# Kernel tuning notes

Measured on AMD Instinct MI355X. Metric: run time of the kernel, lower is better.

Reference implementation:

```python
import math
import jax, jax.numpy as jnp
import numpy as np

B, L, D = 2, 2048, 1024
NH = 16
HS = D // NH
BLOCK_SIZE = 2048


def setup_inputs() -> dict:
    key = jax.random.key(0)
    ks = jax.random.split(key, 4)
    x = jax.random.normal(ks[0], (B, L, D), dtype=jnp.float32)
    Wqkv = jax.random.normal(ks[1], (D, 3 * D), dtype=jnp.float32) * 0.02
    bqkv = jnp.zeros((3 * D,), dtype=jnp.float32)
    Wproj = jax.random.normal(ks[2], (D, D), dtype=jnp.float32) * 0.02
    bproj = jnp.zeros((D,), dtype=jnp.float32)
    Er = jax.random.normal(ks[3], (BLOCK_SIZE, HS), dtype=jnp.float32)
    return {"x": x, "Wqkv": Wqkv, "bqkv": bqkv, "Wproj": Wproj, "bproj": bproj, "Er": Er}


def _skew(QEr):
    # QEr: [B, nh, L, L]  (Music Transformer skew trick)
    b, nh, nr, nc = QEr.shape
    padded = jnp.pad(QEr, ((0, 0), (0, 0), (0, 0), (1, 0)))  # [B, nh, nr, nc+1]
    reshaped = padded.reshape(b, nh, nc + 1, nr)
    return reshaped[:, :, 1:, :]  # [B, nh, nr, nc]


def reference(x, Wqkv, bqkv, Wproj, bproj, Er):
    b, l, d = x.shape
    qkv = x @ Wqkv + bqkv  # [B, L, 3D]
    q, k, v = jnp.split(qkv, 3, axis=2)
    q = q.reshape(b, l, NH, HS).transpose(0, 2, 1, 3)  # [B, nh, L, hs]
    k = k.reshape(b, l, NH, HS).transpose(0, 2, 1, 3)
    v = v.reshape(b, l, NH, HS).transpose(0, 2, 1, 3)

    start = BLOCK_SIZE - l
    Er_t = Er[start:, :].T  # [hs, L]
    QEr = jnp.einsum('bhld,dm->bhlm', q, Er_t)  # [B, nh, L, L]
    Srel = _skew(QEr)

    QK_t = jnp.einsum('bhld,bhmd->bhlm', q, k)
    scale = 1.0 / math.sqrt(HS)
    att = (QK_t + Srel) * scale
    causal = jnp.tril(jnp.ones((l, l), dtype=bool))
    att = jnp.where(causal[None, None, :, :], att, jnp.float32(-jnp.inf))
    att = jax.nn.softmax(att, axis=-1)
    y = jnp.einsum('bhlm,bhmd->bhld', att, v)
    y = y.transpose(0, 2, 1, 3).reshape(b, l, d)
    return y @ Wproj + bproj
```

## Files before the change

### kernel.cpp

```cpp
#include <hip/hip_runtime.h>
#include <stdint.h>

#define BB 2
#define LL 2048
#define DD 1024
#define NHH 16
#define HSS 64

typedef __bf16 bf16x8 __attribute__((ext_vector_type(8)));
typedef float f32x4 __attribute__((ext_vector_type(4)));

__device__ __forceinline__ bf16x8 load8(const float* p) {
  float4 f0 = *(const float4*)p;
  float4 f1 = *(const float4*)(p + 4);
  bf16x8 v;
  v[0] = (__bf16)f0.x; v[1] = (__bf16)f0.y; v[2] = (__bf16)f0.z; v[3] = (__bf16)f0.w;
  v[4] = (__bf16)f1.x; v[5] = (__bf16)f1.y; v[6] = (__bf16)f1.z; v[7] = (__bf16)f1.w;
  return v;
}
__device__ __forceinline__ bf16x8 load8(const __bf16* p) {
  return *(const bf16x8*)p;
}

__device__ __forceinline__ void async_ld16(__bf16* lds_uniform_base,
                                           const __bf16* gptr_per_lane) {
  __builtin_amdgcn_global_load_lds(
      (const __attribute__((address_space(1))) void*)gptr_per_lane,
      (__attribute__((address_space(3))) void*)lds_uniform_base, 16, 0, 0);
}

__global__ void prep_k(const float* __restrict__ Wqkv, const float* __restrict__ x,
                       const float* __restrict__ Er, __bf16* __restrict__ WqkvT,
                       __bf16* __restrict__ xb, __bf16* __restrict__ Erb) {
  int tx = threadIdx.x, ty = threadIdx.y;
  int tid = ty * 32 + tx;
  if (blockIdx.z == 1) {
    if (blockIdx.x >= 2048) return;
    size_t off = ((size_t)blockIdx.x * 256 + tid) * 8;
    *(bf16x8*)&xb[off] = load8(&x[off]);
    return;
  }
  if (blockIdx.z == 2) {
    if (blockIdx.x >= 64) return;
    size_t off = ((size_t)blockIdx.x * 256 + tid) * 8;
    *(bf16x8*)&Erb[off] = load8(&Er[off]);
    return;
  }
  __shared__ __bf16 tile[32][33];
  int c0 = (blockIdx.x % 96) * 32, r0 = (blockIdx.x / 96) * 32;
#pragma unroll
  for (int i = ty; i < 32; i += 8)
    tile[i][tx] = (__bf16)Wqkv[(size_t)(r0 + i) * 3072 + c0 + tx];
  __syncthreads();
#pragma unroll
  for (int i = ty; i < 32; i += 8)
    WqkvT[(size_t)(c0 + i) * 1024 + r0 + tx] = tile[tx][i];
}

__global__ void tconv_k(const float* __restrict__ src, __bf16* __restrict__ dst,
                        int R, int C) {
  __shared__ __bf16 tile[32][33];
  int c0 = blockIdx.x * 32, r0 = blockIdx.y * 32;
  int tx = threadIdx.x, ty = threadIdx.y;
#pragma unroll
  for (int i = ty; i < 32; i += 8)
    tile[i][tx] = (__bf16)src[(size_t)(r0 + i) * C + c0 + tx];
  __syncthreads();
#pragma unroll
  for (int i = ty; i < 32; i += 8)
    dst[(size_t)(c0 + i) * R + r0 + tx] = tile[tx][i];
}

__global__ __launch_bounds__(256) void gemm_qkv_k(
    const __bf16* __restrict__ A, const __bf16* __restrict__ Bt,
    const float* __restrict__ bias, __bf16* __restrict__ Qo,
    __bf16* __restrict__ Ko, __bf16* __restrict__ Vto) {
  const int K = 1024;
  __shared__ __align__(16) __bf16 As[128 * 32];
  __shared__ __align__(16) __bf16 Bs[128 * 32];
  int t = threadIdx.x;
  int wave = t >> 6, lane = t & 63, qd = lane >> 4, lr = lane & 15;
  int m0 = blockIdx.y * 128, n0 = blockIdx.x * 128;
  int wm = (wave >> 1) * 64, wn = (wave & 1) * 64;
  f32x4 acc[4][4] = {};
  int srow = lane >> 2, sch = (lane & 3) * 8;
  const __bf16* Ab[2];
  const __bf16* Bb[2];
#pragma unroll
  for (int c = 0; c < 2; c++) {
    Ab[c] = A + (size_t)(m0 + (wave * 2 + c) * 16 + srow) * K + sch;
    Bb[c] = Bt + (size_t)(n0 + (wave * 2 + c) * 16 + srow) * K + sch;
  }
  for (int k0 = 0; k0 < K; k0 += 32) {
    __syncthreads();
#pragma unroll
    for (int c = 0; c < 2; c++) {
      async_ld16(&As[(wave * 2 + c) * 512], Ab[c] + k0);
      async_ld16(&Bs[(wave * 2 + c) * 512], Bb[c] + k0);
    }
    __syncthreads();
    bf16x8 af[4], bfr[4];
#pragma unroll
    for (int mt = 0; mt < 4; mt++)
      af[mt] = *(const bf16x8*)&As[(wm + mt * 16 + lr) * 32 + qd * 8];
#pragma unroll
    for (int nt = 0; nt < 4; nt++)
      bfr[nt] = *(const bf16x8*)&Bs[(wn + nt * 16 + lr) * 32 + qd * 8];
#pragma unroll
    for (int mt = 0; mt < 4; mt++)
#pragma unroll
      for (int nt = 0; nt < 4; nt++)
        acc[mt][nt] = __builtin_amdgcn_mfma_f32_16x16x32_bf16(af[mt], bfr[nt],
                                                              acc[mt][nt], 0, 0, 0);
  }
  float bvv[4];
#pragma unroll
  for (int nt = 0; nt < 4; nt++) bvv[nt] = bias[n0 + wn + nt * 16 + lr];
#pragma unroll
  for (int mt = 0; mt < 4; mt++)
#pragma unroll
    for (int nt = 0; nt < 4; nt++)
#pragma unroll
      for (int r = 0; r < 4; r++) {
        int row = m0 + wm + mt * 16 + qd * 4 + r;
        int col = n0 + wn + nt * 16 + lr;
        __bf16 bb = (__bf16)(acc[mt][nt][r] + bvv[nt]);
        int b = row >> 11, l = row & 2047;
        int h = (col >> 6) & 15, d = col & 63;
        if (col < DD) {
          Qo[(((size_t)(b * NHH + h)) * LL + l) * HSS + d] = bb;
        } else if (col < 2 * DD) {
          Ko[(((size_t)(b * NHH + h)) * LL + l) * HSS + d] = bb;
        } else {
          Vto[(((size_t)(b * NHH + h)) * HSS + d) * LL + l] = bb;
        }
      }
}

__global__ __launch_bounds__(256) void gemm_proj_k(
    const __bf16* __restrict__ A, const __bf16* __restrict__ Bt,
    const float* __restrict__ bias, float* __restrict__ out) {
  const int K = 1024, N = 1024;
  __shared__ __align__(16) __bf16 As[128 * 32];
  __shared__ __align__(16) __bf16 Bs[64 * 32];
  int t = threadIdx.x;
  int wave = t >> 6, lane = t & 63, qd = lane >> 4, lr = lane & 15;
  int m0 = blockIdx.y * 128, n0 = blockIdx.x * 64;
  int wm = (wave >> 1) * 64, wn = (wave & 1) * 32;
  f32x4 acc[4][2] = {};
  int srow = lane >> 2, sch = (lane & 3) * 8;
  const __bf16* Ab[2];
  const __bf16* Bb;
#pragma unroll
  for (int c = 0; c < 2; c++)
    Ab[c] = A + (size_t)(m0 + (wave * 2 + c) * 16 + srow) * K + sch;
  Bb = Bt + (size_t)(n0 + wave * 16 + srow) * K + sch;

  for (int k0 = 0; k0 < K; k0 += 32) {
    __syncthreads();
#pragma unroll
    for (int c = 0; c < 2; c++)
      async_ld16(&As[(wave * 2 + c) * 512], Ab[c] + k0);
    async_ld16(&Bs[wave * 512], Bb + k0);
    __syncthreads();
    bf16x8 af[4], bfr[2];
#pragma unroll
    for (int mt = 0; mt < 4; mt++)
      af[mt] = *(const bf16x8*)&As[(wm + mt * 16 + lr) * 32 + qd * 8];
#pragma unroll
    for (int nt = 0; nt < 2; nt++)
      bfr[nt] = *(const bf16x8*)&Bs[(wn + nt * 16 + lr) * 32 + qd * 8];
#pragma unroll
    for (int mt = 0; mt < 4; mt++)
#pragma unroll
      for (int nt = 0; nt < 2; nt++)
        acc[mt][nt] = __builtin_amdgcn_mfma_f32_16x16x32_bf16(af[mt], bfr[nt],
                                                              acc[mt][nt], 0, 0, 0);
  }
  float bvv[2];
#pragma unroll
  for (int nt = 0; nt < 2; nt++) bvv[nt] = bias[n0 + wn + nt * 16 + lr];
#pragma unroll
  for (int mt = 0; mt < 4; mt++)
#pragma unroll
    for (int nt = 0; nt < 2; nt++)
#pragma unroll
      for (int r = 0; r < 4; r++) {
        int row = m0 + wm + mt * 16 + qd * 4 + r;
        int col = n0 + wn + nt * 16 + lr;
        out[(size_t)row * N + col] = acc[mt][nt][r] + bvv[nt];
      }
}

__global__ __launch_bounds__(256, 3) void flash_k(
    const __bf16* __restrict__ Qg, const __bf16* __restrict__ Kg,
    const __bf16* __restrict__ Vtg, const __bf16* __restrict__ Erb,
    __bf16* __restrict__ Po0, __bf16* __restrict__ Po1,
    float* __restrict__ Lp0, float* __restrict__ Lp1) {
  __shared__ __align__(16) __bf16 Kld[64 * 72];
  __shared__ __align__(16) __bf16 Vld[64 * 72];
  __shared__ __align__(16) __bf16 Pball[4][16 * 72];

  int bh = blockIdx.x;
  int tile = 31 - (int)blockIdx.y;
  int i0 = tile * 64;
  int niter = tile + 1;
  int mid = (niter + 1) >> 1;
  int it0 = (blockIdx.z == 0) ? 0 : mid;
  int it1 = (blockIdx.z == 0) ? mid : niter;
  const __bf16* Qh = Qg + (size_t)bh * LL * HSS;
  const __bf16* Kh = Kg + (size_t)bh * LL * HSS;
  const __bf16* Vth = Vtg + (size_t)bh * HSS * LL;
  int b = bh >> 4, h = bh & 15;
  int t = threadIdx.x, wave = t >> 6, lane = t & 63, qd = lane >> 4, lr = lane & 15;
  __bf16* Pb = &Pball[wave][0];
  int cbase = 48 - wave * 16;

  bf16x8 bones;
#pragma unroll
  for (int q = 0; q < 8; q++) bones[q] = (lr == 0) ? (__bf16)1.f : (__bf16)0.f;

  int jj = t >> 2, hf = t & 3;

  bf16x8 aq[2];
  {
    const __bf16* qrow = Qh + (size_t)(i0 + wave * 16 + lr) * HSS + qd * 8;
    aq[0] = *(const bf16x8*)qrow;
    aq[1] = *(const bf16x8*)(qrow + 32);
  }
  f32x4 oacc[5] = {};

  bf16x8 kr0, kr1, vr0, vr1;
  auto prefetch = [&](int j0) {
    kr0 = *(const bf16x8*)&Kh[(size_t)(j0 + jj) * HSS + hf * 16];
    kr1 = *(const bf16x8*)&Kh[(size_t)(j0 + jj) * HSS + hf * 16 + 8];
    vr0 = *(const bf16x8*)&Vth[(size_t)jj * LL + j0 + hf * 16];
    vr1 = *(const bf16x8*)&Vth[(size_t)jj * LL + j0 + hf * 16 + 8];
  };
  if (it0 < it1) prefetch(it0 * 64);

  for (int it = it0; it < it1; ++it) {
    int j0 = it * 64;
    __syncthreads();
    *(bf16x8*)&Kld[jj * 72 + hf * 16] = kr0;
    *(bf16x8*)&Kld[jj * 72 + hf * 16 + 8] = kr1;
    *(bf16x8*)&Vld[jj * 72 + hf * 16] = vr0;
    *(bf16x8*)&Vld[jj * 72 + hf * 16 + 8] = vr1;
    __syncthreads();
    if (it + 1 < it1) prefetch((it + 1) * 64);

    bf16x8 ef[5][2];
    int ebase = LL - 64 - i0 + j0 + cbase;
#pragma unroll
    for (int ct = 0; ct < 5; ct++) {
      int e = ebase + ct * 16 + lr;
      e = (e < LL) ? e : (LL - 1);
#pragma unroll
      for (int kc = 0; kc < 2; kc++)
        ef[ct][kc] = *(const bf16x8*)&Erb[(size_t)e * HSS + kc * 32 + qd * 8];
    }

    f32x4 sacc[4] = {};
#pragma unroll
    for (int ct = 0; ct < 4; ct++)
#pragma unroll
      for (int kc = 0; kc < 2; kc++) {
        bf16x8 bk = *(const bf16x8*)&Kld[(ct * 16 + lr) * 72 + kc * 32 + qd * 8];
        sacc[ct] = __builtin_amdgcn_mfma_f32_16x16x32_bf16(aq[kc], bk, sacc[ct], 0, 0, 0);
      }
    f32x4 racc[5] = {};
#pragma unroll
    for (int ct = 0; ct < 5; ct++)
#pragma unroll
      for (int kc = 0; kc < 2; kc++)
        racc[ct] = __builtin_amdgcn_mfma_f32_16x16x32_bf16(aq[kc], ef[ct][kc],
                                                           racc[ct], 0, 0, 0);

#pragma unroll
    for (int r = 0; r < 4; r++) {
      int tr = qd * 4 + r;
      int base = 15 - tr + lr;
      int src = qd * 16 + (base & 15);
      int hi = base >> 4;
      float sh[5];
#pragma unroll
      for (int ct = 0; ct < 5; ct++) sh[ct] = __shfl(racc[ct][r], src, 64);
      int gi = i0 + wave * 16 + tr;
#pragma unroll
      for (int ct2 = 0; ct2 < 4; ct2++) {
        float rel = hi ? sh[ct2 + 1] : sh[ct2];
        float s = (sacc[ct2][r] + rel) * 0.125f;
        int gj = j0 + ct2 * 16 + lr;
        float p = (gj <= gi) ? __expf(s) : 0.f;
        Pb[tr * 72 + ct2 * 16 + lr] = (__bf16)p;
      }
    }

    bf16x8 ap0 = *(const bf16x8*)&Pb[lr * 72 + qd * 8];
    bf16x8 ap1 = *(const bf16x8*)&Pb[lr * 72 + 32 + qd * 8];
#pragma unroll
    for (int dt = 0; dt < 4; dt++) {
      bf16x8 bv0 = *(const bf16x8*)&Vld[(dt * 16 + lr) * 72 + qd * 8];
      bf16x8 bv1 = *(const bf16x8*)&Vld[(dt * 16 + lr) * 72 + 32 + qd * 8];
      oacc[dt] = __builtin_amdgcn_mfma_f32_16x16x32_bf16(ap0, bv0, oacc[dt], 0, 0, 0);
      oacc[dt] = __builtin_amdgcn_mfma_f32_16x16x32_bf16(ap1, bv1, oacc[dt], 0, 0, 0);
    }
    oacc[4] = __builtin_amdgcn_mfma_f32_16x16x32_bf16(ap0, bones, oacc[4], 0, 0, 0);
    oacc[4] = __builtin_amdgcn_mfma_f32_16x16x32_bf16(ap1, bones, oacc[4], 0, 0, 0);
  }

  __bf16* Po = (blockIdx.z == 0) ? Po0 : Po1;
  float* Lp = (blockIdx.z == 0) ? Lp0 : Lp1;
#pragma unroll
  for (int r = 0; r < 4; r++) {
    int l = i0 + wave * 16 + qd * 4 + r;
    if (lr == 0) Lp[(size_t)bh * LL + l] = oacc[4][r];
#pragma unroll
    for (int dt = 0; dt < 4; dt++) {
      int d = dt * 16 + lr;
      Po[((size_t)(b * LL) + l) * DD + h * HSS + d] = (__bf16)oacc[dt][r];
    }
  }
}

__global__ void combine_k(const __bf16* __restrict__ Po0,
                          const __bf16* __restrict__ Po1,
                          const float* __restrict__ Lp0,
                          const float* __restrict__ Lp1,
                          __bf16* __restrict__ Y) {
  size_t f = ((size_t)blockIdx.x * 256 + threadIdx.x) * 8;
  int dfull = (int)(f & 1023);
  int h = dfull >> 6;
  int l = (int)((f >> 10) & 2047);
  int b = (int)(f >> 21);
  size_t lidx = ((size_t)(b * NHH + h)) * LL + l;
  float linv = 1.f / (Lp0[lidx] + Lp1[lidx]);
  bf16x8 a = *(const bf16x8*)&Po0[f];
  bf16x8 c = *(const bf16x8*)&Po1[f];
  bf16x8 o;
#pragma unroll
  for (int q = 0; q < 8; q++)
    o[q] = (__bf16)(((float)a[q] + (float)c[q]) * linv);
  *(bf16x8*)&Y[f] = o;
}

extern "C" void kernel_launch(void* const* d_in, const int* in_sizes, int n_in,
                              void* d_out, int out_size, void* d_ws, size_t ws_size,
                              hipStream_t stream) {
  const float* x = (const float*)d_in[0];
  const float* Wqkv = (const float*)d_in[1];
  const float* bqkv = (const float*)d_in[2];
  const float* Wproj = (const float*)d_in[3];
  const float* bproj = (const float*)d_in[4];
  const float* Er = (const float*)d_in[5];
  float* out = (float*)d_out;

  if (ws_size < 4u * 8388608u) return;

  uint8_t* w = (uint8_t*)d_ws;
  __bf16* Q = (__bf16*)w;  w += (size_t)BB * NHH * LL * HSS * 2;
  __bf16* Kt = (__bf16*)w; w += (size_t)BB * NHH * LL * HSS * 2;
  __bf16* Vt = (__bf16*)w; w += (size_t)BB * NHH * LL * HSS * 2;
  __bf16* Y = (__bf16*)w;  w += (size_t)BB * LL * DD * 2;

  __bf16* WqkvT = (__bf16*)d_out;
  __bf16* xb = (__bf16*)((uint8_t*)d_out + (size_t)3072 * 1024 * 2);
  __bf16* Erb = (__bf16*)((uint8_t*)d_out + (size_t)3072 * 1024 * 2 + (size_t)4096 * 1024 * 2);
  __bf16* Po1 = (__bf16*)d_out;
  float* Lp0 = (float*)((uint8_t*)d_out + (size_t)BB * LL * DD * 2);
  float* Lp1 = (float*)((uint8_t*)d_out + (size_t)BB * LL * DD * 2 + (size_t)BB * NHH * LL * 4);
  __bf16* Po0 = Y;
  __bf16* WprojT = Q;

  prep_k<<<dim3(3072, 1, 3), dim3(32, 8), 0, stream>>>(Wqkv, x, Er, WqkvT, xb, Erb);
  gemm_qkv_k<<<dim3(3072 / 128, 4096 / 128), 256, 0, stream>>>(
      xb, WqkvT, bqkv, Q, Kt, Vt);
  flash_k<<<dim3(BB * NHH, 32, 2), 256, 0, stream>>>(
      Q, Kt, Vt, Erb, Po0, Po1, Lp0, Lp1);
  combine_k<<<dim3(2048), 256, 0, stream>>>(Po0, Po1, Lp0, Lp1, Y);
  tconv_k<<<dim3(1024 / 32, 1024 / 32), dim3(32, 8), 0, stream>>>(Wproj, WprojT, 1024, 1024);
  gemm_proj_k<<<dim3(1024 / 64, 4096 / 128), 256, 0, stream>>>(Y, WprojT, bproj, out);
}
```

Measured before the change: 251.2 us.

## Tune flash kernel occupancy, hoist index math, use exp2 and setprio around MFMAs

Raises the launch-bounds occupancy hint from 3 to 4 blocks per CU. Hoists the per-row shuffle indices, masks and LDS offsets out of the loop and replaces __shfl with a direct ds_bpermute. Uses exp2 with a prescaled log2e constant and splits the Er loads into two halves so they interleave with the QK MFMAs. Wraps the MFMA groups in s_setprio. The tighter register budget from the higher occupancy hint may cause spills.

```diff
diff --git a/kernel.cpp b/kernel.cpp
--- a/kernel.cpp
+++ b/kernel.cpp
@@ -192,7 +192,7 @@
       }
 }
 
-__global__ __launch_bounds__(256, 3) void flash_k(
+__global__ __launch_bounds__(256, 4) void flash_k(
     const __bf16* __restrict__ Qg, const __bf16* __restrict__ Kg,
     const __bf16* __restrict__ Vtg, const __bf16* __restrict__ Erb,
     __bf16* __restrict__ Po0, __bf16* __restrict__ Po1,
@@ -216,11 +216,24 @@
   __bf16* Pb = &Pball[wave][0];
   int cbase = 48 - wave * 16;
 
+  const float SC = 0.18033688011112042f;
+
   bf16x8 bones;
 #pragma unroll
   for (int q = 0; q < 8; q++) bones[q] = (lr == 0) ? (__bf16)1.f : (__bf16)0.f;
 
   int jj = t >> 2, hf = t & 3;
+
+  int idx4[4], hiv[4], pbv[4], giv[4];
+#pragma unroll
+  for (int r = 0; r < 4; r++) {
+    int tr = qd * 4 + r;
+    int base = 15 - tr + lr;
+    idx4[r] = (qd * 16 + (base & 15)) << 2;
+    hiv[r] = base >> 4;
+    pbv[r] = tr * 72 + lr;
+    giv[r] = i0 + wave * 16 + tr;
+  }
 
   bf16x8 aq[2];
   {
@@ -249,18 +262,20 @@
     __syncthreads();
     if (it + 1 < it1) prefetch((it + 1) * 64);
 
-    bf16x8 ef[5][2];
-    int ebase = LL - 64 - i0 + j0 + cbase;
+    int ebase = LL - 64 - i0 + j0 + cbase + lr;
+    int e[5];
 #pragma unroll
     for (int ct = 0; ct < 5; ct++) {
-      int e = ebase + ct * 16 + lr;
-      e = (e < LL) ? e : (LL - 1);
-#pragma unroll
-      for (int kc = 0; kc < 2; kc++)
-        ef[ct][kc] = *(const bf16x8*)&Erb[(size_t)e * HSS + kc * 32 + qd * 8];
+      int v = ebase + ct * 16;
+      e[ct] = (v < LL) ? v : (LL - 1);
     }
+    bf16x8 ef0[5];
+#pragma unroll
+    for (int ct = 0; ct < 5; ct++)
+      ef0[ct] = *(const bf16x8*)&Erb[(size_t)e[ct] * HSS + qd * 8];
 
     f32x4 sacc[4] = {};
+    __builtin_amdgcn_s_setprio(1);
 #pragma unroll
     for (int ct = 0; ct < 4; ct++)
 #pragma unroll
@@ -268,36 +283,43 @@
         bf16x8 bk = *(const bf16x8*)&Kld[(ct * 16 + lr) * 72 + kc * 32 + qd * 8];
         sacc[ct] = __builtin_amdgcn_mfma_f32_16x16x32_bf16(aq[kc], bk, sacc[ct], 0, 0, 0);
       }
+    __builtin_amdgcn_s_setprio(0);
+
+    bf16x8 ef1[5];
+#pragma unroll
+    for (int ct = 0; ct < 5; ct++)
+      ef1[ct] = *(const bf16x8*)&Erb[(size_t)e[ct] * HSS + 32 + qd * 8];
+
     f32x4 racc[5] = {};
+    __builtin_amdgcn_s_setprio(1);
 #pragma unroll
     for (int ct = 0; ct < 5; ct++)
-#pragma unroll
-      for (int kc = 0; kc < 2; kc++)
-        racc[ct] = __builtin_amdgcn_mfma_f32_16x16x32_bf16(aq[kc], ef[ct][kc],
-                                                           racc[ct], 0, 0, 0);
+      racc[ct] = __builtin_amdgcn_mfma_f32_16x16x32_bf16(aq[0], ef0[ct], racc[ct], 0, 0, 0);
+#pragma unroll
+    for (int ct = 0; ct < 5; ct++)
+      racc[ct] = __builtin_amdgcn_mfma_f32_16x16x32_bf16(aq[1], ef1[ct], racc[ct], 0, 0, 0);
+    __builtin_amdgcn_s_setprio(0);
 
 #pragma unroll
     for (int r = 0; r < 4; r++) {
-      int tr = qd * 4 + r;
-      int base = 15 - tr + lr;
-      int src = qd * 16 + (base & 15);
-      int hi = base >> 4;
       float sh[5];
 #pragma unroll
-      for (int ct = 0; ct < 5; ct++) sh[ct] = __shfl(racc[ct][r], src, 64);
-      int gi = i0 + wave * 16 + tr;
+      for (int ct = 0; ct < 5; ct++)
+        sh[ct] = __int_as_float(
+            __builtin_amdgcn_ds_bpermute(idx4[r], __float_as_int(racc[ct][r])));
+      int di = giv[r] - j0;
 #pragma unroll
       for (int ct2 = 0; ct2 < 4; ct2++) {
-        float rel = hi ? sh[ct2 + 1] : sh[ct2];
-        float s = (sacc[ct2][r] + rel) * 0.125f;
-        int gj = j0 + ct2 * 16 + lr;
-        float p = (gj <= gi) ? __expf(s) : 0.f;
-        Pb[tr * 72 + ct2 * 16 + lr] = (__bf16)p;
+        float rel = hiv[r] ? sh[ct2 + 1] : sh[ct2];
+        float p = __builtin_exp2f((sacc[ct2][r] + rel) * SC);
+        p = (ct2 * 16 + lr <= di) ? p : 0.f;
+        Pb[pbv[r] + ct2 * 16] = (__bf16)p;
       }
     }
 
     bf16x8 ap0 = *(const bf16x8*)&Pb[lr * 72 + qd * 8];
     bf16x8 ap1 = *(const bf16x8*)&Pb[lr * 72 + 32 + qd * 8];
+    __builtin_amdgcn_s_setprio(1);
 #pragma unroll
     for (int dt = 0; dt < 4; dt++) {
       bf16x8 bv0 = *(const bf16x8*)&Vld[(dt * 16 + lr) * 72 + qd * 8];
@@ -307,6 +329,7 @@
     }
     oacc[4] = __builtin_amdgcn_mfma_f32_16x16x32_bf16(ap0, bones, oacc[4], 0, 0, 0);
     oacc[4] = __builtin_amdgcn_mfma_f32_16x16x32_bf16(ap1, bones, oacc[4], 0, 0, 0);
+    __builtin_amdgcn_s_setprio(0);
   }
 
   __bf16* Po = (blockIdx.z == 0) ? Po0 : Po1;
```

After: 306.1 us. 21.9% more time.
